# Kernel optimization log

Measured on AMD Instinct MI355X. Metric: run time of the kernel, lower is better.

Reference implementation:

```python
import jax, jax.numpy as jnp
import numpy as np

IN_F, OUT_F, GROUP = 4096, 11008, 128
N_GROUPS = IN_F // GROUP  # 32 (in_features divisible by group_size -> no padding)


def setup_inputs() -> dict:
    key = jax.random.key(0)
    kx, kw, ks, kb = jax.random.split(key, 4)
    x = jax.random.normal(kx, (4, 2048, IN_F), dtype=jnp.float32)
    weight_q = jax.random.randint(kw, (OUT_F, IN_F), -128, 128, dtype=jnp.int32).astype(jnp.int8)
    scales = jax.random.uniform(ks, (OUT_F, N_GROUPS), dtype=jnp.float32) * 0.01 + 1e-4
    bias = jax.random.normal(kb, (OUT_F,), dtype=jnp.float32)
    return {"x": x, "weight_q": weight_q, "scales": scales, "bias": bias}


def reference(x, weight_q, scales, bias):
    # Dequantize: group-wise scale along in_features, cast to fp16 (as torch .half())
    W = (weight_q.astype(jnp.float32).reshape(OUT_F, N_GROUPS, GROUP)
         * scales[:, :, None]).reshape(OUT_F, IN_F).astype(jnp.float16)
    # fp16 linear: y = x W^T + b, then back to fp32
    y = jnp.einsum('bsi,oi->bso', x.astype(jnp.float16), W) + bias.astype(jnp.float16)
    return y.astype(jnp.float32)
```

## Files before the change

kernel.cpp:

```cpp
#include <hip/hip_runtime.h>

#define IN_F 4096
#define OUT_F 11008
#define NGROUPS 32
#define M_TOTAL 8192
#define BM 256
#define BN 256
#define BK 32
#define NKT (IN_F / BK)

typedef _Float16 half_t;
typedef unsigned short ushort_t;
typedef __attribute__((ext_vector_type(8))) short short8;
typedef __attribute__((ext_vector_type(4))) float f32x4;
typedef __attribute__((ext_vector_type(4))) int i32x4;
typedef __attribute__((ext_vector_type(4))) unsigned short us4;

typedef __attribute__((address_space(1))) const void gvoid_t;
typedef __attribute__((address_space(3))) void lvoid_t;

__device__ __forceinline__ unsigned short f32_to_bf16_rne(float f) {
  unsigned int u = __builtin_bit_cast(unsigned int, f);
  u += 0x7FFFu + ((u >> 16) & 1u);
  return (unsigned short)(u >> 16);
}

__global__ void convert_x_k(const float* __restrict__ x, ushort_t* __restrict__ xh) {
  const int n4 = M_TOTAL * IN_F / 4;
  int stride = gridDim.x * blockDim.x;
  for (int i = blockIdx.x * blockDim.x + threadIdx.x; i < n4; i += stride) {
    f32x4 v = __builtin_nontemporal_load((const f32x4*)x + i);
    us4 h;
    h[0] = f32_to_bf16_rne(v[0]);
    h[1] = f32_to_bf16_rne(v[1]);
    h[2] = f32_to_bf16_rne(v[2]);
    h[3] = f32_to_bf16_rne(v[3]);
    ((us4*)xh)[i] = h;
  }
}

__global__ void dequant_w_k(const int* __restrict__ wq,
                            const float* __restrict__ scales,
                            ushort_t* __restrict__ wh) {
  int row = blockIdx.x;
  int t = threadIdx.x;
  size_t base = (size_t)row * IN_F + (size_t)t * 8;
  float s = scales[row * NGROUPS + (t >> 4)];
  i32x4 q0 = __builtin_nontemporal_load((const i32x4*)(wq + base));
  i32x4 q1 = __builtin_nontemporal_load((const i32x4*)(wq + base) + 1);
  us4 h0, h1;
#pragma unroll
  for (int j = 0; j < 4; ++j) h0[j] = f32_to_bf16_rne((float)q0[j] * s);
#pragma unroll
  for (int j = 0; j < 4; ++j) h1[j] = f32_to_bf16_rne((float)q1[j] * s);
  *(us4*)(wh + base) = h0;
  *(us4*)(wh + base + 4) = h1;
}


#define BAR() __builtin_amdgcn_s_barrier()
#define SB0() __builtin_amdgcn_sched_barrier(0)
#define PRIO1() __builtin_amdgcn_s_setprio(1)
#define PRIO0() __builtin_amdgcn_s_setprio(0)
#define VMCNT(N) asm volatile("s_waitcnt vmcnt(" #N ")" ::: "memory")
#define LGKM(N) asm volatile("s_waitcnt lgkmcnt(" #N ")" ::: "memory")

#define GLD(G, D) __builtin_amdgcn_global_load_lds((gvoid_t*)(G), (lvoid_t*)(D), 16, 0, 0)

#define STAGE(KT, S)                                                       \
  do {                                                                     \
    const half_t* gA_ = pAsrc + (KT) * 32;                                 \
    const half_t* gB_ = pBsrc + (KT) * 32;                                 \
    char* dA_ = (char*)&lds[S][0][0] + t16;                                \
    char* dB_ = (char*)&lds[S][1][0] + t16;                                \
    GLD(gA_, dA_);                                                         \
    GLD(gA_ + 128 * IN_F, dA_ + 8192);                                     \
    GLD(gB_, dB_);                                                         \
    GLD(gB_ + 128 * IN_F, dB_ + 8192);                                     \
  } while (0)

#define RDS(AA, BB, S)                                                     \
  do {                                                                     \
    const char* Ab_ = (const char*)&lds[S][0][0];                          \
    const char* Bb_ = (const char*)&lds[S][1][0];                          \
    _Pragma("unroll") for (int m_ = 0; m_ < 8; ++m_)                       \
        AA[m_] = *(const short8*)(Ab_ + aoff + m_ * 1024);                 \
    _Pragma("unroll") for (int n_ = 0; n_ < 4; ++n_)                       \
        BB[n_] = *(const short8*)(Bb_ + boff + n_ * 1024);                 \
  } while (0)

#define MFMA_ALL(AA, BB)                                                   \
  do {                                                                     \
    _Pragma("unroll") for (int m_ = 0; m_ < 8; ++m_)                       \
        _Pragma("unroll") for (int n_ = 0; n_ < 4; ++n_)                   \
            acc[m_][n_] = __builtin_amdgcn_mfma_f32_16x16x32_bf16(         \
                AA[m_], BB[n_], acc[m_][n_], 0, 0, 0);                     \
  } while (0)

#define PH(RA_, RB_, RSLOT, STKT, SSLOT, MA_, MB_, FEN)                    \
  do {                                                                     \
    RDS(RA_, RB_, RSLOT);                                                  \
    STAGE(STKT, SSLOT);                                                    \
    LGKM(12); SB0(); PRIO1();                                              \
    MFMA_ALL(MA_, MB_);                                                    \
    PRIO0();                                                               \
    if ((FEN) == 4) VMCNT(4);                                              \
    BAR(); SB0();                                                          \
  } while (0)

#define PHN(RA_, RB_, RSLOT, MA_, MB_, FEN)                                \
  do {                                                                     \
    RDS(RA_, RB_, RSLOT);                                                  \
    LGKM(12); SB0(); PRIO1();                                              \
    MFMA_ALL(MA_, MB_);                                                    \
    PRIO0();                                                               \
    if ((FEN) == 0) VMCNT(0);                                              \
    BAR(); SB0();                                                          \
  } while (0)

__global__ __launch_bounds__(512, 1) void gemm_k(const half_t* __restrict__ A,
                                                 const half_t* __restrict__ B,
                                                 const float* __restrict__ bias,
                                                 float* __restrict__ C) {
  __shared__ __align__(16) half_t lds[4][2][8192];

  const int tid = threadIdx.x;
  const int lane = tid & 63;
  const int wv = tid >> 6;
  const int wm = wv >> 2;
  const int wn = wv & 3;
  const int t16 = tid * 16;

  const int nwg = gridDim.x;
  const int perx = nwg >> 3;
  const int L = ((int)blockIdx.x & 7) * perx + ((int)blockIdx.x >> 3);
  const int band = L >> 7;
  const int rr_ = L & 127;
  const int bn0 = band << 2;
  const int cols = (43 - bn0) < 4 ? (43 - bn0) : 4;
  const int bm = rr_ / cols;
  const int bn = bn0 + rr_ % cols;
  const int row0 = bm * BM;
  const int col0 = bn * BN;

  const int c16 = (tid & 3) * 16;
  const int srow = tid >> 2;
  const int clog = c16 ^ ((srow & 6) << 3);
  const int kidx = clog >> 1;
  const half_t* pAsrc = A + (size_t)(row0 + srow) * IN_F + kidx;
  const half_t* pBsrc = B + (size_t)(col0 + srow) * IN_F + kidx;

  const int r16 = lane & 15;
  const int kg = lane >> 4;
  const int aoff = (wm * 128 + r16) * 64 + ((kg * 16) ^ ((r16 & 6) << 3));
  const int boff = (wn * 64 + r16) * 64 + ((kg * 16) ^ ((r16 & 6) << 3));

  f32x4 acc[8][4];
#pragma unroll
  for (int m = 0; m < 8; ++m)
#pragma unroll
    for (int n = 0; n < 4; ++n) acc[m][n] = (f32x4){0.f, 0.f, 0.f, 0.f};

  short8 aA[8], bA[4], aB[8], bB[4];

  STAGE(0, 0);
  STAGE(1, 1);
  STAGE(2, 2);
  VMCNT(4);
  BAR();
  SB0();
  RDS(aA, bA, 0);

  for (int u = 0; u < 62; ++u) {
    const int t0 = 2 * u;
    PH(aB, bB, (t0 + 1) & 3, t0 + 3, (t0 + 3) & 3, aA, bA, 4);
    PH(aA, bA, (t0 + 2) & 3, t0 + 4, (t0 + 4) & 3, aB, bB, 4);
  }
  PH(aB, bB, 1, 127, 3, aA, bA, 4);
  PHN(aA, bA, 2, aB, bB, 0);
  PHN(aB, bB, 3, aA, bA, -1);
  LGKM(0);
  SB0();
  MFMA_ALL(aB, bB);

  const int kg4 = kg * 4;
#pragma unroll
  for (int nf = 0; nf < 4; ++nf) {
    int col = col0 + wn * 64 + nf * 16 + r16;
    _Float16 bh = (_Float16)bias[col];
#pragma unroll
    for (int mf = 0; mf < 8; ++mf) {
      int rb = row0 + wm * 128 + mf * 16 + kg4;
#pragma unroll
      for (int r = 0; r < 4; ++r) {
        _Float16 v = (_Float16)acc[mf][nf][r] + bh;
        __builtin_nontemporal_store((float)v, &C[(size_t)(rb + r) * OUT_F + col]);
      }
    }
  }
}

__global__ void naive_k(const float* __restrict__ x, const int* __restrict__ wq,
                        const float* __restrict__ scales, const float* __restrict__ bias,
                        float* __restrict__ out) {
  long idx = (long)blockIdx.x * blockDim.x + threadIdx.x;
  if (idx >= (long)M_TOTAL * OUT_F) return;
  int m = (int)(idx / OUT_F);
  int n = (int)(idx % OUT_F);
  float acc = 0.f;
  for (int g = 0; g < NGROUPS; ++g) {
    float s = scales[n * NGROUPS + g];
    for (int k = g * 128; k < (g + 1) * 128; ++k) {
      _Float16 xv = (_Float16)x[(size_t)m * IN_F + k];
      _Float16 wv = (_Float16)((float)wq[(size_t)n * IN_F + k] * s);
      acc += (float)xv * (float)wv;
    }
  }
  _Float16 r = (_Float16)acc + (_Float16)bias[n];
  out[idx] = (float)r;
}

extern "C" void kernel_launch(void* const* d_in, const int* in_sizes, int n_in,
                              void* d_out, int out_size, void* d_ws, size_t ws_size,
                              hipStream_t stream) {
  const float* x = (const float*)d_in[0];
  const int* wq = (const int*)d_in[1];
  const float* scales = (const float*)d_in[2];
  const float* bias = (const float*)d_in[3];
  float* out = (float*)d_out;

  const size_t xh_bytes = (size_t)M_TOTAL * IN_F * 2;
  const size_t wh_bytes = (size_t)OUT_F * IN_F * 2;

  if (ws_size >= xh_bytes + wh_bytes) {
    ushort_t* xh = (ushort_t*)d_ws;
    ushort_t* wh = (ushort_t*)((char*)d_ws + xh_bytes);
    convert_x_k<<<2048, 256, 0, stream>>>(x, xh);
    dequant_w_k<<<OUT_F, 512, 0, stream>>>(wq, scales, wh);
    gemm_k<<<(M_TOTAL / BM) * (OUT_F / BN), 512, 0, stream>>>(
        (const half_t*)xh, (const half_t*)wh, bias, out);
  } else {
    long total = (long)M_TOTAL * OUT_F;
    naive_k<<<(int)((total + 255) / 256), 256, 0, stream>>>(x, wq, scales, bias, out);
  }
}
```

Before: 724.1 us.

## Stagger wave halves so LDS reads and MFMA phases interleave across waves

Splits the eight waves into two groups with different phase orderings. The first four waves issue LDS reads and global staging before their MFMAs. The other four run MFMAs first and then issue reads and staging. The goal is to spread LDS and VMEM traffic across each barrier interval so matrix-core work from one group overlaps memory instructions from the other. The cost is a divergent code path, which roughly doubles code size, and a risk of mismatched barrier or vmcnt accounting between the two groups.

Measured after the change: 718.2 us. Within noise of the previous version (-0.8%).

```diff
diff --git a/kernel.cpp b/kernel.cpp
--- a/kernel.cpp
+++ b/kernel.cpp
@@ -97,25 +97,23 @@
                 AA[m_], BB[n_], acc[m_][n_], 0, 0, 0);                     \
   } while (0)
 
-#define PH(RA_, RB_, RSLOT, STKT, SSLOT, MA_, MB_, FEN)                    \
+#define PH0(RA_, RB_, RSLOT, STKT, SSLOT, MA_, MB_)                        \
   do {                                                                     \
     RDS(RA_, RB_, RSLOT);                                                  \
     STAGE(STKT, SSLOT);                                                    \
     LGKM(12); SB0(); PRIO1();                                              \
     MFMA_ALL(MA_, MB_);                                                    \
-    PRIO0();                                                               \
-    if ((FEN) == 4) VMCNT(4);                                              \
-    BAR(); SB0();                                                          \
-  } while (0)
-
-#define PHN(RA_, RB_, RSLOT, MA_, MB_, FEN)                                \
-  do {                                                                     \
-    RDS(RA_, RB_, RSLOT);                                                  \
-    LGKM(12); SB0(); PRIO1();                                              \
+    PRIO0(); VMCNT(4); BAR(); SB0();                                       \
+  } while (0)
+
+#define PH1(RA_, RB_, RSLOT, STKT, SSLOT, MA_, MB_)                        \
+  do {                                                                     \
+    LGKM(0); SB0(); PRIO1();                                               \
     MFMA_ALL(MA_, MB_);                                                    \
     PRIO0();                                                               \
-    if ((FEN) == 0) VMCNT(0);                                              \
-    BAR(); SB0();                                                          \
+    RDS(RA_, RB_, RSLOT);                                                  \
+    STAGE(STKT, SSLOT);                                                    \
+    VMCNT(4); BAR(); SB0();                                                \
   } while (0)
 
 __global__ __launch_bounds__(512, 1) void gemm_k(const half_t* __restrict__ A,
@@ -171,17 +169,37 @@
   SB0();
   RDS(aA, bA, 0);
 
-  for (int u = 0; u < 62; ++u) {
-    const int t0 = 2 * u;
-    PH(aB, bB, (t0 + 1) & 3, t0 + 3, (t0 + 3) & 3, aA, bA, 4);
-    PH(aA, bA, (t0 + 2) & 3, t0 + 4, (t0 + 4) & 3, aB, bB, 4);
-  }
-  PH(aB, bB, 1, 127, 3, aA, bA, 4);
-  PHN(aA, bA, 2, aB, bB, 0);
-  PHN(aB, bB, 3, aA, bA, -1);
-  LGKM(0);
-  SB0();
-  MFMA_ALL(aB, bB);
+  if (wv < 4) {
+    for (int u = 0; u < 62; ++u) {
+      const int t0 = 2 * u;
+      PH0(aB, bB, (t0 + 1) & 3, t0 + 3, (t0 + 3) & 3, aA, bA);
+      PH0(aA, bA, (t0 + 2) & 3, t0 + 4, (t0 + 4) & 3, aB, bB);
+    }
+    PH0(aB, bB, 1, 127, 3, aA, bA);
+    RDS(aA, bA, 2);
+    LGKM(12); SB0(); PRIO1(); MFMA_ALL(aB, bB); PRIO0();
+    VMCNT(0); BAR(); SB0();
+    RDS(aB, bB, 3);
+    LGKM(12); SB0(); PRIO1(); MFMA_ALL(aA, bA); PRIO0();
+    BAR(); SB0();
+    LGKM(0); SB0();
+    MFMA_ALL(aB, bB);
+  } else {
+    for (int u = 0; u < 62; ++u) {
+      const int t0 = 2 * u;
+      PH1(aB, bB, (t0 + 1) & 3, t0 + 3, (t0 + 3) & 3, aA, bA);
+      PH1(aA, bA, (t0 + 2) & 3, t0 + 4, (t0 + 4) & 3, aB, bB);
+    }
+    PH1(aB, bB, 1, 127, 3, aA, bA);
+    LGKM(0); SB0(); PRIO1(); MFMA_ALL(aB, bB); PRIO0();
+    RDS(aA, bA, 2);
+    VMCNT(0); BAR(); SB0();
+    LGKM(0); SB0(); PRIO1(); MFMA_ALL(aA, bA); PRIO0();
+    RDS(aB, bB, 3);
+    BAR(); SB0();
+    LGKM(0); SB0();
+    MFMA_ALL(aB, bB);
+  }
 
   const int kg4 = kg * 4;
 #pragma unroll
```

## Load B fragments directly from global into registers, stage only A in LDS

Applied to the files above, without the earlier changes.

The GEMM main loop now reads the B (weight) operand per-wave directly from global memory into registers, one step ahead, instead of staging it through LDS. Only A is staged through LDS, using a double-buffered layout with two K-halves per buffer. A-fragment reads are split into two halves so MFMAs on the first half can start while the second half is still arriving. This cuts LDS traffic and footprint, but adds uncoalesced-ish global loads for B with latency exposed in registers, and B rows are redundantly fetched across the two wm waves.

Result: slower. 1.127 ms (+55.6%).

```diff
diff --git a/kernel.cpp b/kernel.cpp
--- a/kernel.cpp
+++ b/kernel.cpp
@@ -7,7 +7,7 @@
 #define BM 256
 #define BN 256
 #define BK 32
-#define NKT (IN_F / BK)
+#define NPH 128
 
 typedef _Float16 half_t;
 typedef unsigned short ushort_t;
@@ -64,72 +64,60 @@
 #define PRIO0() __builtin_amdgcn_s_setprio(0)
 #define VMCNT(N) asm volatile("s_waitcnt vmcnt(" #N ")" ::: "memory")
 #define LGKM(N) asm volatile("s_waitcnt lgkmcnt(" #N ")" ::: "memory")
-
 #define GLD(G, D) __builtin_amdgcn_global_load_lds((gvoid_t*)(G), (lvoid_t*)(D), 16, 0, 0)
 
-#define STAGE(KT, S)                                                       \
-  do {                                                                     \
-    const half_t* gA_ = pAsrc + (KT) * 32;                                 \
-    const half_t* gB_ = pBsrc + (KT) * 32;                                 \
-    char* dA_ = (char*)&lds[S][0][0] + t16;                                \
-    char* dB_ = (char*)&lds[S][1][0] + t16;                                \
-    GLD(gA_, dA_);                                                         \
-    GLD(gA_ + 128 * IN_F, dA_ + 8192);                                     \
-    GLD(gB_, dB_);                                                         \
-    GLD(gB_ + 128 * IN_F, dB_ + 8192);                                     \
+#define ALDS(S, KH) (smem + (S) * 32768 + (KH) * 16384)
+
+#define LOADB(BSET, KOFF)                                                      \
+  _Pragma("unroll") for (int n_ = 0; n_ < 4; ++n_)                             \
+      BSET[n_] = *(const short8*)(pB + (size_t)n_ * 16 * IN_F + (KOFF));
+
+#define STAGEA(KOFF, S, KH)                                                    \
+  do {                                                                         \
+    const half_t* g_ = pAsrc + (KOFF);                                         \
+    char* d_ = ALDS(S, KH) + tid * 16;                                         \
+    GLD(g_, d_);                                                               \
+    GLD(g_ + 128 * IN_F, d_ + 8192);                                           \
   } while (0)
 
-#define RDS(AA, BB, S)                                                     \
-  do {                                                                     \
-    const char* Ab_ = (const char*)&lds[S][0][0];                          \
-    const char* Bb_ = (const char*)&lds[S][1][0];                          \
-    _Pragma("unroll") for (int m_ = 0; m_ < 8; ++m_)                       \
-        AA[m_] = *(const short8*)(Ab_ + aoff + m_ * 1024);                 \
-    _Pragma("unroll") for (int n_ = 0; n_ < 4; ++n_)                       \
-        BB[n_] = *(const short8*)(Bb_ + boff + n_ * 1024);                 \
-  } while (0)
-
-#define MFMA_ALL(AA, BB)                                                   \
-  do {                                                                     \
-    _Pragma("unroll") for (int m_ = 0; m_ < 8; ++m_)                       \
-        _Pragma("unroll") for (int n_ = 0; n_ < 4; ++n_)                   \
-            acc[m_][n_] = __builtin_amdgcn_mfma_f32_16x16x32_bf16(         \
-                AA[m_], BB[n_], acc[m_][n_], 0, 0, 0);                     \
-  } while (0)
-
-#define PH(RA_, RB_, RSLOT, STKT, SSLOT, MA_, MB_, FEN)                    \
-  do {                                                                     \
-    RDS(RA_, RB_, RSLOT);                                                  \
-    STAGE(STKT, SSLOT);                                                    \
-    LGKM(12); SB0(); PRIO1();                                              \
-    MFMA_ALL(MA_, MB_);                                                    \
-    PRIO0();                                                               \
-    if ((FEN) == 4) VMCNT(4);                                              \
-    BAR(); SB0();                                                          \
-  } while (0)
-
-#define PHN(RA_, RB_, RSLOT, MA_, MB_, FEN)                                \
-  do {                                                                     \
-    RDS(RA_, RB_, RSLOT);                                                  \
-    LGKM(12); SB0(); PRIO1();                                              \
-    MFMA_ALL(MA_, MB_);                                                    \
-    PRIO0();                                                               \
-    if ((FEN) == 0) VMCNT(0);                                              \
-    BAR(); SB0();                                                          \
+#define MFMA_H(ASET, BSET, MH)                                                 \
+  _Pragma("unroll") for (int i_ = 0; i_ < 4; ++i_)                             \
+      _Pragma("unroll") for (int j_ = 0; j_ < 4; ++j_)                         \
+          acc[(MH)*4 + i_][j_] = __builtin_amdgcn_mfma_f32_16x16x32_bf16(      \
+              ASET[i_], BSET[j_], acc[(MH)*4 + i_][j_], 0, 0, 0);
+
+#define PHASE(S, KH, BCUR, BNXT, BLD, KOFFB, STG, KOFFS, FEN)                  \
+  do {                                                                         \
+    const char* Ab_ = ALDS(S, KH);                                             \
+    _Pragma("unroll") for (int m_ = 0; m_ < 4; ++m_)                           \
+        a0[m_] = *(const short8*)(Ab_ + aoff + m_ * 1024);                     \
+    SB0();                                                                     \
+    _Pragma("unroll") for (int m_ = 0; m_ < 4; ++m_)                           \
+        a1[m_] = *(const short8*)(Ab_ + aoff + 4096 + m_ * 1024);              \
+    if (BLD) { LOADB(BNXT, KOFFB); }                                           \
+    if (STG) { STAGEA(KOFFS, (S) ^ 1, KH); }                                   \
+    LGKM(4); SB0(); PRIO1();                                                   \
+    MFMA_H(a0, BCUR, 0);                                                       \
+    LGKM(0); SB0();                                                            \
+    MFMA_H(a1, BCUR, 1);                                                       \
+    PRIO0();                                                                   \
+    if ((FEN) == 6) VMCNT(6);                                                  \
+    if ((FEN) == 4) VMCNT(4);                                                  \
+    if ((FEN) == 0) VMCNT(0);                                                  \
+    BAR(); SB0();                                                              \
   } while (0)
 
 __global__ __launch_bounds__(512, 1) void gemm_k(const half_t* __restrict__ A,
                                                  const half_t* __restrict__ B,
                                                  const float* __restrict__ bias,
                                                  float* __restrict__ C) {
-  __shared__ __align__(16) half_t lds[4][2][8192];
+  __shared__ __align__(16) char smem[65536];
 
   const int tid = threadIdx.x;
   const int lane = tid & 63;
   const int wv = tid >> 6;
   const int wm = wv >> 2;
   const int wn = wv & 3;
-  const int t16 = tid * 16;
 
   const int nwg = gridDim.x;
   const int perx = nwg >> 3;
@@ -148,12 +136,11 @@
   const int clog = c16 ^ ((srow & 6) << 3);
   const int kidx = clog >> 1;
   const half_t* pAsrc = A + (size_t)(row0 + srow) * IN_F + kidx;
-  const half_t* pBsrc = B + (size_t)(col0 + srow) * IN_F + kidx;
 
   const int r16 = lane & 15;
   const int kg = lane >> 4;
   const int aoff = (wm * 128 + r16) * 64 + ((kg * 16) ^ ((r16 & 6) << 3));
-  const int boff = (wn * 64 + r16) * 64 + ((kg * 16) ^ ((r16 & 6) << 3));
+  const half_t* pB = B + (size_t)(col0 + wn * 64 + r16) * IN_F + kg * 8;
 
   f32x4 acc[8][4];
 #pragma unroll
@@ -161,27 +148,23 @@
 #pragma unroll
     for (int n = 0; n < 4; ++n) acc[m][n] = (f32x4){0.f, 0.f, 0.f, 0.f};
 
-  short8 aA[8], bA[4], aB[8], bB[4];
-
-  STAGE(0, 0);
-  STAGE(1, 1);
-  STAGE(2, 2);
+  short8 a0[4], a1[4], bA[4], bB[4];
+
+  STAGEA(0, 0, 0);
+  STAGEA(32, 0, 1);
+  LOADB(bA, 0);
   VMCNT(4);
   BAR();
   SB0();
-  RDS(aA, bA, 0);
-
-  for (int u = 0; u < 62; ++u) {
-    const int t0 = 2 * u;
-    PH(aB, bB, (t0 + 1) & 3, t0 + 3, (t0 + 3) & 3, aA, bA, 4);
-    PH(aA, bA, (t0 + 2) & 3, t0 + 4, (t0 + 4) & 3, aB, bB, 4);
-  }
-  PH(aB, bB, 1, 127, 3, aA, bA, 4);
-  PHN(aA, bA, 2, aB, bB, 0);
-  PHN(aB, bB, 3, aA, bA, -1);
-  LGKM(0);
-  SB0();
-  MFMA_ALL(aB, bB);
+
+  for (int u = 0; u < 63; ++u) {
+    const int p0 = 2 * u;
+    const int s = u & 1;
+    PHASE(s, 0, bA, bB, 1, (p0 + 1) * 32, 1, (p0 + 2) * 32, 6);
+    PHASE(s, 1, bB, bA, 1, (p0 + 2) * 32, 1, (p0 + 3) * 32, 6);
+  }
+  PHASE(1, 0, bA, bB, 1, 127 * 32, 0, 0, 4);
+  PHASE(1, 1, bB, bA, 0, 0, 0, 0, 0);
 
   const int kg4 = kg * 4;
 #pragma unroll
```
